# Optimization experiments

Hardware: AMD Instinct MI355X
Metric: run time of the kernel (lower is better)

## Reference

```python
import jax, jax.numpy as jnp
import numpy as np

N = 50000      # nodes
E = 800000     # edges
IN = 16        # node_features_size
OUT = 32       # conv out channels
HID = 25       # edge-MLP hidden
C = 10         # num_classes


def setup_inputs() -> dict:
    key = jax.random.key(0)
    ks = jax.random.split(key, 12)
    inp = {
        "x": jax.random.normal(ks[0], (N, IN), dtype=jnp.float32),
        "edge_attr": jax.random.uniform(ks[1], (E, 1), dtype=jnp.float32),
        "edge_index": jax.random.randint(ks[2], (2, E), 0, N, dtype=jnp.int64),
        # edge-MLP nn1: Linear(1,25) -> ReLU -> Linear(25, IN*OUT)
        "w1": jax.random.normal(ks[3], (1, HID), dtype=jnp.float32) * (1.0 / np.sqrt(1)),
        "b1": jnp.zeros((HID,), dtype=jnp.float32),
        "w2": jax.random.normal(ks[4], (HID, IN * OUT), dtype=jnp.float32) * (1.0 / np.sqrt(HID)),
        "b2": jnp.zeros((IN * OUT,), dtype=jnp.float32),
        # NNConv root weight and bias
        "root": jax.random.normal(ks[5], (IN, OUT), dtype=jnp.float32) * (1.0 / np.sqrt(IN)),
        "bias": jnp.zeros((OUT,), dtype=jnp.float32),
        # fc1: Linear(32, C)
        "fc_w": jax.random.normal(ks[6], (OUT, C), dtype=jnp.float32) * (1.0 / np.sqrt(OUT)),
        "fc_b": jnp.zeros((C,), dtype=jnp.float32),
    }
    return inp


def reference(x, edge_attr, edge_index, w1, b1, w2, b2, root, bias, fc_w, fc_b):
    src = edge_index[0]  # message sources (x_j)
    dst = edge_index[1]  # aggregation targets (x_i)
    # edge MLP -> per-edge weight matrices [E, IN, OUT]
    h = jax.nn.relu(edge_attr @ w1 + b1)
    w_e = (h @ w2 + b2).reshape(-1, IN, OUT)
    # gather source features, per-edge matmul
    msg = jnp.einsum('ei,eio->eo', x[src], w_e)  # [E, OUT]
    # scatter-max aggregation to destination nodes
    agg = jax.ops.segment_max(msg, dst, num_segments=N)
    agg = jnp.where(jnp.isfinite(agg), agg, 0.0)  # empty segments -> 0
    # root transform + bias, then ELU and classifier
    out = jax.nn.elu(agg + x @ root + bias)
    logits = out @ fc_w + fc_b
    return jax.nn.log_softmax(logits, axis=1)
```

## Files before the change

kernel.cpp:

```cpp
#include <hip/hip_runtime.h>
#include <hip/hip_bf16.h>
#include <stdint.h>

#define NN   50000
#define NE   800000
#define INF_ 16
#define OUTF 32
#define HIDN 25
#define NC   10
#define QG   2048
#define QPB  16
#define DPB  16
#define NB   3125
#define EPB  4096
#define NBLK 196
#define ASTR 33
#define ECAP 768
#define SCH  13

#define SENT 0x007FFFFFu

#define GB_PQ   98
#define GB_HIST NBLK
#define GB_G2   128
#define GB_XH   391

typedef _Float16 f16x2 __attribute__((ext_vector_type(2)));

__device__ __forceinline__ uint32_t map_f(float f) {
    uint32_t b = __float_as_uint(f);
    return (b & 0x80000000u) ? ~b : (b | 0x80000000u);
}
__device__ __forceinline__ float unmap_f(uint32_t u) {
    return (u & 0x80000000u) ? __uint_as_float(u ^ 0x80000000u)
                             : __uint_as_float(~u);
}
__device__ __forceinline__ float f16lo(uint32_t u) {
    union { uint16_t s; _Float16 h; } v; v.s = (uint16_t)(u & 0xFFFF);
    return (float)v.h;
}
__device__ __forceinline__ float f16hi(uint32_t u) {
    union { uint16_t s; _Float16 h; } v; v.s = (uint16_t)(u >> 16);
    return (float)v.h;
}
__device__ __forceinline__ uint32_t packf16(float a, float b) {
    union { uint32_t u; f16x2 h; } p;
    p.h[0] = (_Float16)a; p.h[1] = (_Float16)b;
    return p.u;
}
__device__ __forceinline__ float dot2f(uint32_t g, uint32_t xb, float acc) {
#if __has_builtin(__builtin_amdgcn_fdot2)
    union { uint32_t u; f16x2 h; } ug, ux;
    ug.u = g; ux.u = xb;
    return __builtin_amdgcn_fdot2(ug.h, ux.h, acc, false);
#else
    return fmaf(f16lo(g), f16lo(xb), fmaf(f16hi(g), f16hi(xb), acc));
#endif
}

__global__ __launch_bounds__(64) void flag_k(const float* __restrict__ w1,
                                             const float* __restrict__ b1,
                                             uint32_t* __restrict__ flagw) {
    if (threadIdx.x == 0) {
        uint32_t flag = 1, mask = 0;
        for (int k = 0; k < HIDN; ++k) {
            float w = w1[k], b = b1[k];
            if (w != 0.f) {
                float t = -b / w;
                if (t > 0.f && t < 1.f) flag = 0;
            }
            if (fmaf(0.5f, w, b) > 0.f) mask |= (1u << k);
        }
        flagw[0] = flag;
        flagw[1] = mask;
    }
}

__global__ __launch_bounds__(256) void prep_k(const float* __restrict__ w1,
                                              const float* __restrict__ b1,
                                              const float* __restrict__ w2,
                                              const float* __restrict__ b2,
                                              const float* __restrict__ x,
                                              const int* __restrict__ ei,
                                              const uint32_t* __restrict__ flagw,
                                              uint32_t* __restrict__ PQ,
                                              uint32_t* __restrict__ G2,
                                              uint32_t* __restrict__ xh,
                                              uint32_t* __restrict__ H) {
    __shared__ union {
        struct {
            float w2s[HIDN * 512];
            float b2s[512];
            float ca[512];
            float cb[512];
            float hs[QPB][HIDN];
        } g;
        uint32_t hloc[NB];
    } sm;

    const int b = blockIdx.x;
    if (b < GB_PQ) {
        for (int i = threadIdx.x; i < HIDN * 512; i += 256) sm.g.w2s[i] = w2[i];
        for (int i = threadIdx.x; i < 512; i += 256) sm.g.b2s[i] = b2[i];
        __syncthreads();
        const uint32_t mask = flagw[1];
        for (int e = threadIdx.x; e < 512; e += 256) {
            float ca = sm.g.b2s[e], cb = 0.f;
            for (int k = 0; k < HIDN; ++k) {
                if ((mask >> k) & 1u) {
                    float wv = sm.g.w2s[k * 512 + e];
                    ca = fmaf(b1[k], wv, ca);
                    cb = fmaf(w1[k], wv, cb);
                }
            }
            sm.g.ca[e] = ca;
            sm.g.cb[e] = cb;
        }
        __syncthreads();
        for (int rep = 0; rep < 2; ++rep) {
            int n = b * 512 + rep * 256 + threadIdx.x;
            if (n < NN) {
                float xv[INF_];
                const float* xr = x + (size_t)n * INF_;
#pragma unroll
                for (int i = 0; i < INF_; i += 4) {
                    float4 v = *reinterpret_cast<const float4*>(xr + i);
                    xv[i] = v.x; xv[i+1] = v.y; xv[i+2] = v.z; xv[i+3] = v.w;
                }
                float P[OUTF], Q[OUTF];
#pragma unroll
                for (int o = 0; o < OUTF; ++o) {
                    float p = 0.f, q = 0.f;
#pragma unroll
                    for (int i = 0; i < INF_; ++i) {
                        p = fmaf(xv[i], sm.g.ca[i * 32 + o], p);
                        q = fmaf(xv[i], sm.g.cb[i * 32 + o], q);
                    }
                    P[o] = p; Q[o] = q;
                }
                uint32_t* row = PQ + (size_t)n * 32;
#pragma unroll
                for (int j = 0; j < 16; ++j) row[j] = packf16(P[2*j], P[2*j+1]);
#pragma unroll
                for (int j = 0; j < 16; ++j) row[16+j] = packf16(Q[2*j], Q[2*j+1]);
            }
        }
    } else if (b < GB_PQ + GB_HIST) {
        const int blk = b - GB_PQ;
        for (int i = threadIdx.x; i < NB; i += 256) sm.hloc[i] = 0;
        __syncthreads();
        const int base = blk * EPB;
        for (int j = 0; j < EPB; j += 256) {
            int e = base + j + threadIdx.x;
            if (e < NE) atomicAdd(&sm.hloc[ei[NE + e] >> 4], 1u);
        }
        __syncthreads();
        for (int i = threadIdx.x; i < NB; i += 256)
            H[(size_t)i * NBLK + blk] = sm.hloc[i];
    } else if (b < GB_PQ + GB_HIST + GB_G2) {
        if (flagw[0] == 1u) return;
        const int gb = b - GB_PQ - GB_HIST;
        for (int i = threadIdx.x; i < HIDN * 512; i += 256) sm.g.w2s[i] = w2[i];
        for (int i = threadIdx.x; i < 512; i += 256) sm.g.b2s[i] = b2[i];
        for (int i = threadIdx.x; i < QPB * HIDN; i += 256) {
            int qq = i / HIDN, k = i - qq * HIDN;
            float aq = (gb * QPB + qq + 0.5f) * (1.0f / (float)QG);
            sm.g.hs[qq][k] = fmaxf(fmaf(aq, w1[k], b1[k]), 0.f);
        }
        __syncthreads();
        for (int qq = 0; qq < QPB; ++qq) {
            const int q = gb * QPB + qq;
            int e = threadIdx.x;
            int ip = e >> 5, o = e & 31;
            float g0 = sm.g.b2s[(2 * ip) * OUTF + o];
            float g1 = sm.g.b2s[(2 * ip + 1) * OUTF + o];
#pragma unroll
            for (int k = 0; k < HIDN; ++k) {
                float h = sm.g.hs[qq][k];
                g0 = fmaf(h, sm.g.w2s[k * 512 + (2 * ip) * OUTF + o], g0);
                g1 = fmaf(h, sm.g.w2s[k * 512 + (2 * ip + 1) * OUTF + o], g1);
            }
            G2[(size_t)q * 256 + e] = packf16(g0, g1);
        }
    } else {
        if (flagw[0] == 1u) return;
        int t4 = ((b - GB_PQ - GB_HIST - GB_G2) * 256 + threadIdx.x) * 4;
        if (t4 < NN * INF_ / 2) {
            const float4* xp = reinterpret_cast<const float4*>(x) + (t4 >> 1);
            float4 va = xp[0];
            float4 vb = xp[1];
            xh[t4]     = packf16(va.x, va.y);
            xh[t4 + 1] = packf16(va.z, va.w);
            xh[t4 + 2] = packf16(vb.x, vb.y);
            xh[t4 + 3] = packf16(vb.z, vb.w);
        }
    }
}

__global__ __launch_bounds__(256) void colsum_k(const uint32_t* __restrict__ H,
                                                uint32_t* __restrict__ Bp,
                                                uint32_t* __restrict__ tot) {
    const int bin  = (blockIdx.x * 256 + threadIdx.x) >> 6;
    const int lane = threadIdx.x & 63;
    if (bin >= NB) return;
    const uint32_t* hr = H + (size_t)bin * NBLK;
    uint32_t* br = Bp + (size_t)bin * NBLK;
    uint32_t carry = 0;
    for (int b0 = 0; b0 < NBLK; b0 += 64) {
        int b = b0 + lane;
        uint32_t v = (b < NBLK) ? hr[b] : 0;
        uint32_t inc = v;
#pragma unroll
        for (int off = 1; off < 64; off <<= 1) {
            uint32_t t = __shfl_up(inc, off);
            if (lane >= off) inc += t;
        }
        if (b < NBLK) br[b] = carry + inc - v;
        carry += __shfl(inc, 63);
    }
    if (lane == 0) tot[bin] = carry;
}

__global__ __launch_bounds__(256) void binscan_k(const uint32_t* __restrict__ tot,
                                                 uint32_t* __restrict__ bstart) {
    __shared__ uint32_t part[256];
    const int t = threadIdx.x;
    uint32_t loc[SCH];
    uint32_t s = 0;
#pragma unroll
    for (int j = 0; j < SCH; ++j) {
        int idx = t * SCH + j;
        uint32_t v = (idx < NB) ? tot[idx] : 0;
        loc[j] = s;
        s += v;
    }
    part[t] = s;
    __syncthreads();
    for (int off = 1; off < 256; off <<= 1) {
        uint32_t add = (t >= off) ? part[t - off] : 0;
        __syncthreads();
        part[t] += add;
        __syncthreads();
    }
    uint32_t base = (t > 0) ? part[t - 1] : 0;
#pragma unroll
    for (int j = 0; j < SCH; ++j) {
        int idx = t * SCH + j;
        if (idx < NB) bstart[idx] = base + loc[j];
    }
    if (t == 255) bstart[NB] = part[255];
}

__global__ __launch_bounds__(256) void scatter_k(const int* __restrict__ ei,
                                                 const float* __restrict__ ea,
                                                 const uint32_t* __restrict__ Bp,
                                                 const uint32_t* __restrict__ bstart,
                                                 uint2* __restrict__ sorted) {
    __shared__ uint32_t cur[NB];
    for (int i = threadIdx.x; i < NB; i += 256) cur[i] = 0;
    __syncthreads();
    const int base = blockIdx.x * EPB;
    for (int j = 0; j < EPB; j += 256) {
        int e = base + j + threadIdx.x;
        if (e < NE) {
            int sn = ei[e];
            int d  = ei[NE + e];
            float a = ea[e];
            int bin = d >> 4;
            uint32_t r = atomicAdd(&cur[bin], 1u);
            uint32_t pos = bstart[bin] + Bp[(size_t)bin * NBLK + blockIdx.x] + r;
            sorted[pos] = make_uint2(__float_as_uint(a),
                                     ((uint32_t)sn << 4) | (uint32_t)(d & 15));
        }
    }
}

__global__ __launch_bounds__(256) void fused_k(const uint2* __restrict__ sorted,
                                               const uint32_t* __restrict__ bstart,
                                               const uint32_t* __restrict__ flagw,
                                               const float* __restrict__ x,
                                               const uint32_t* __restrict__ PQ,
                                               const uint32_t* __restrict__ xh,
                                               const uint32_t* __restrict__ G2,
                                               const float* __restrict__ root,
                                               const float* __restrict__ bias,
                                               const float* __restrict__ fcw,
                                               const float* __restrict__ fcb,
                                               float* __restrict__ out) {
    __shared__ uint2    ebuf[ECAP];
    __shared__ uint32_t agg[DPB * ASTR];
    __shared__ float rs[INF_ * OUTF];
    __shared__ float bs[OUTF];
    __shared__ float fws[OUTF * NC];
    __shared__ float fbs[NC];

    const int bin  = blockIdx.x;
    const int segs = (int)bstart[bin];
    const int cnt  = (int)bstart[bin + 1] - segs;
    const int scnt = cnt < ECAP ? cnt : ECAP;

    for (int i = threadIdx.x; i < scnt; i += 256) ebuf[i] = sorted[segs + i];
    for (int i = threadIdx.x; i < DPB * ASTR; i += 256) agg[i] = SENT;
    for (int i = threadIdx.x; i < INF_ * OUTF; i += 256) rs[i] = root[i];
    if (threadIdx.x < OUTF) bs[threadIdx.x] = bias[threadIdx.x];
    for (int i = threadIdx.x; i < OUTF * NC; i += 256) fws[i] = fcw[i];
    if (threadIdx.x < NC) fbs[threadIdx.x] = fcb[threadIdx.x];
    const uint32_t flag = flagw[0];
    __syncthreads();

    const int c   = threadIdx.x & 7;
    const int grp = threadIdx.x >> 3;

    if (flag) {
        int it = grp;
        for (; it + 32 < cnt; it += 64) {
            uint2 rA = (it < ECAP) ? ebuf[it] : sorted[segs + it];
            int itB = it + 32;
            uint2 rB = (itB < ECAP) ? ebuf[itB] : sorted[segs + itB];
            float aA = __uint_as_float(rA.x), aB = __uint_as_float(rB.x);
            int sA = rA.y >> 4, sB = rB.y >> 4;
            int dA = rA.y & 15, dB = rB.y & 15;
            const uint2* pA = reinterpret_cast<const uint2*>(PQ + (size_t)sA * 32);
            const uint2* pB = reinterpret_cast<const uint2*>(PQ + (size_t)sB * 32);
            uint2 PuA = pA[c], QuA = pA[8 + c];
            uint2 PuB = pB[c], QuB = pB[8 + c];

            float a0 = fmaf(aA, f16lo(QuA.x), f16lo(PuA.x));
            float a1 = fmaf(aA, f16hi(QuA.x), f16hi(PuA.x));
            float a2 = fmaf(aA, f16lo(QuA.y), f16lo(PuA.y));
            float a3 = fmaf(aA, f16hi(QuA.y), f16hi(PuA.y));
            float b0 = fmaf(aB, f16lo(QuB.x), f16lo(PuB.x));
            float b1v = fmaf(aB, f16hi(QuB.x), f16hi(PuB.x));
            float b2v = fmaf(aB, f16lo(QuB.y), f16lo(PuB.y));
            float b3 = fmaf(aB, f16hi(QuB.y), f16hi(PuB.y));

            uint32_t* agA = &agg[dA * ASTR + c * 4];
            atomicMax(&agA[0], map_f(a0));
            atomicMax(&agA[1], map_f(a1));
            atomicMax(&agA[2], map_f(a2));
            atomicMax(&agA[3], map_f(a3));
            uint32_t* agB = &agg[dB * ASTR + c * 4];
            atomicMax(&agB[0], map_f(b0));
            atomicMax(&agB[1], map_f(b1v));
            atomicMax(&agB[2], map_f(b2v));
            atomicMax(&agB[3], map_f(b3));
        }
        if (it < cnt) {
            uint2 rA = (it < ECAP) ? ebuf[it] : sorted[segs + it];
            float aA = __uint_as_float(rA.x);
            int sA = rA.y >> 4;
            int dA = rA.y & 15;
            const uint2* pA = reinterpret_cast<const uint2*>(PQ + (size_t)sA * 32);
            uint2 PuA = pA[c], QuA = pA[8 + c];
            float a0 = fmaf(aA, f16lo(QuA.x), f16lo(PuA.x));
            float a1 = fmaf(aA, f16hi(QuA.x), f16hi(PuA.x));
            float a2 = fmaf(aA, f16lo(QuA.y), f16lo(PuA.y));
            float a3 = fmaf(aA, f16hi(QuA.y), f16hi(PuA.y));
            uint32_t* agA = &agg[dA * ASTR + c * 4];
            atomicMax(&agA[0], map_f(a0));
            atomicMax(&agA[1], map_f(a1));
            atomicMax(&agA[2], map_f(a2));
            atomicMax(&agA[3], map_f(a3));
        }
    } else {
        for (int it = grp; it < cnt; it += 32) {
            uint2 rec = (it < ECAP) ? ebuf[it] : sorted[segs + it];
            float a = __uint_as_float(rec.x);
            int src = rec.y >> 4;
            int db  = rec.y & 15;
            int q = (int)(a * (float)QG);
            q = q < 0 ? 0 : (q > QG - 1 ? QG - 1 : q);
            const uint4* xp = reinterpret_cast<const uint4*>(xh) + src * 2;
            uint4 hx0 = xp[0];
            uint4 hx1 = xp[1];
            const uint4* gq = reinterpret_cast<const uint4*>(G2) + (size_t)q * 64 + c;
            uint4 g0 = gq[0],  g1 = gq[8],  g2 = gq[16], g3 = gq[24];
            uint4 g4 = gq[32], g5 = gq[40], g6 = gq[48], g7 = gq[56];
            float p0 = 0.f, p1 = 0.f, p2 = 0.f, p3 = 0.f;
            p0 = dot2f(g0.x, hx0.x, p0); p1 = dot2f(g0.y, hx0.x, p1);
            p2 = dot2f(g0.z, hx0.x, p2); p3 = dot2f(g0.w, hx0.x, p3);
            p0 = dot2f(g1.x, hx0.y, p0); p1 = dot2f(g1.y, hx0.y, p1);
            p2 = dot2f(g1.z, hx0.y, p2); p3 = dot2f(g1.w, hx0.y, p3);
            p0 = dot2f(g2.x, hx0.z, p0); p1 = dot2f(g2.y, hx0.z, p1);
            p2 = dot2f(g2.z, hx0.z, p2); p3 = dot2f(g2.w, hx0.z, p3);
            p0 = dot2f(g3.x, hx0.w, p0); p1 = dot2f(g3.y, hx0.w, p1);
            p2 = dot2f(g3.z, hx0.w, p2); p3 = dot2f(g3.w, hx0.w, p3);
            p0 = dot2f(g4.x, hx1.x, p0); p1 = dot2f(g4.y, hx1.x, p1);
            p2 = dot2f(g4.z, hx1.x, p2); p3 = dot2f(g4.w, hx1.x, p3);
            p0 = dot2f(g5.x, hx1.y, p0); p1 = dot2f(g5.y, hx1.y, p1);
            p2 = dot2f(g5.z, hx1.y, p2); p3 = dot2f(g5.w, hx1.y, p3);
            p0 = dot2f(g6.x, hx1.z, p0); p1 = dot2f(g6.y, hx1.z, p1);
            p2 = dot2f(g6.z, hx1.z, p2); p3 = dot2f(g6.w, hx1.z, p3);
            p0 = dot2f(g7.x, hx1.w, p0); p1 = dot2f(g7.y, hx1.w, p1);
            p2 = dot2f(g7.z, hx1.w, p2); p3 = dot2f(g7.w, hx1.w, p3);
            uint32_t* ag = &agg[db * ASTR + c * 4];
            atomicMax(&ag[0], map_f(p0));
            atomicMax(&ag[1], map_f(p1));
            atomicMax(&ag[2], map_f(p2));
            atomicMax(&ag[3], map_f(p3));
        }
    }
    __syncthreads();

    {
        const int li8 = threadIdx.x & 7;
        const int dl  = threadIdx.x >> 3;
        const int n   = bin * DPB + dl;
        if (dl < DPB && n < NN) {
            const uint32_t* ar = &agg[dl * ASTR + li8 * 4];
            float av[4];
#pragma unroll
            for (int qq = 0; qq < 4; ++qq) {
                uint32_t u = ar[qq];
                av[qq] = (u == SENT) ? 0.f : unmap_f(u);
            }
            const float* xr = x + (size_t)n * INF_;
            float4 xa = *reinterpret_cast<const float4*>(xr);
            float4 xb = *reinterpret_cast<const float4*>(xr + 4);
            float4 xc = *reinterpret_cast<const float4*>(xr + 8);
            float4 xd = *reinterpret_cast<const float4*>(xr + 12);
            float xv[INF_] = {xa.x,xa.y,xa.z,xa.w, xb.x,xb.y,xb.z,xb.w,
                              xc.x,xc.y,xc.z,xc.w, xd.x,xd.y,xd.z,xd.w};
            float ov[4];
#pragma unroll
            for (int qq = 0; qq < 4; ++qq) {
                int oc = li8 * 4 + qq;
                float tv = av[qq] + bs[oc];
#pragma unroll
                for (int i = 0; i < INF_; ++i) tv = fmaf(xv[i], rs[i * OUTF + oc], tv);
                ov[qq] = (tv > 0.f) ? tv : expm1f(tv);
            }
            float lg[NC];
#pragma unroll
            for (int cc = 0; cc < NC; ++cc) {
                float tv = 0.f;
#pragma unroll
                for (int qq = 0; qq < 4; ++qq) tv = fmaf(ov[qq], fws[(li8 * 4 + qq) * NC + cc], tv);
                lg[cc] = tv;
            }
#pragma unroll
            for (int m = 1; m <= 4; m <<= 1) {
#pragma unroll
                for (int cc = 0; cc < NC; ++cc) lg[cc] += __shfl_xor(lg[cc], m);
            }
#pragma unroll
            for (int cc = 0; cc < NC; ++cc) lg[cc] += fbs[cc];

            float mx = lg[0];
#pragma unroll
            for (int cc = 1; cc < NC; ++cc) mx = fmaxf(mx, lg[cc]);
            float ssum = 0.f;
#pragma unroll
            for (int cc = 0; cc < NC; ++cc) ssum += expf(lg[cc] - mx);
            float lse = mx + logf(ssum);

            float* orow = out + (size_t)n * NC;
            orow[li8] = lg[li8] - lse;
            if (li8 < 2) orow[8 + li8] = lg[8 + li8] - lse;
        }
    }
}

extern "C" void kernel_launch(void* const* d_in, const int* in_sizes, int n_in,
                              void* d_out, int out_size, void* d_ws, size_t ws_size,
                              hipStream_t stream) {
    const float* x    = (const float*)d_in[0];
    const float* ea   = (const float*)d_in[1];
    const int*   ei   = (const int*)d_in[2];
    const float* w1   = (const float*)d_in[3];
    const float* b1   = (const float*)d_in[4];
    const float* w2   = (const float*)d_in[5];
    const float* b2   = (const float*)d_in[6];
    const float* root = (const float*)d_in[7];
    const float* bias = (const float*)d_in[8];
    const float* fcw  = (const float*)d_in[9];
    const float* fcb  = (const float*)d_in[10];
    float* out = (float*)d_out;

    size_t off = 0;
    auto alloc = [&](size_t bytes) {
        void* p = (char*)d_ws + off;
        off += (bytes + 255) & ~(size_t)255;
        return p;
    };
    uint32_t* flagw    = (uint32_t*)alloc(256);
    uint32_t* PQ       = (uint32_t*)alloc((size_t)NN * 32 * 4);
    uint32_t* G2       = (uint32_t*)alloc((size_t)QG * 256 * 4);
    uint32_t* xh       = (uint32_t*)alloc((size_t)NN * INF_ * 2);
    uint32_t* H        = (uint32_t*)alloc((size_t)NB * NBLK * 4);
    uint32_t* Bp       = (uint32_t*)alloc((size_t)NB * NBLK * 4);
    uint32_t* tot      = (uint32_t*)alloc((size_t)NB * 4);
    uint32_t* bstart   = (uint32_t*)alloc((size_t)(NB + 1) * 4);
    uint2*    sorted   = (uint2*)alloc((size_t)NE * 8);

    flag_k<<<1, 64, 0, stream>>>(w1, b1, flagw);
    prep_k<<<GB_PQ + GB_HIST + GB_G2 + GB_XH, 256, 0, stream>>>(
        w1, b1, w2, b2, x, ei, flagw, PQ, G2, xh, H);
    colsum_k<<<(NB * 64 + 255) / 256, 256, 0, stream>>>(H, Bp, tot);
    binscan_k<<<1, 256, 0, stream>>>(tot, bstart);
    scatter_k<<<NBLK, 256, 0, stream>>>(ei, ea, Bp, bstart, sorted);
    fused_k<<<NB, 256, 0, stream>>>(sorted, bstart, flagw, x, PQ, xh, G2,
                                    root, bias, fcw, fcb, out);
}
```

Before: 86.78 us.

## Inline flag computation, drop flag kernel, and spread PQ precompute over more blocks

```diff
diff --git a/kernel.cpp b/kernel.cpp
--- a/kernel.cpp
+++ b/kernel.cpp
@@ -20,7 +20,7 @@
 
 #define SENT 0x007FFFFFu
 
-#define GB_PQ   98
+#define GB_PQ   1563
 #define GB_HIST NBLK
 #define GB_G2   128
 #define GB_XH   391
@@ -58,22 +58,16 @@
 #endif
 }
 
-__global__ __launch_bounds__(64) void flag_k(const float* __restrict__ w1,
-                                             const float* __restrict__ b1,
-                                             uint32_t* __restrict__ flagw) {
-    if (threadIdx.x == 0) {
-        uint32_t flag = 1, mask = 0;
-        for (int k = 0; k < HIDN; ++k) {
-            float w = w1[k], b = b1[k];
-            if (w != 0.f) {
-                float t = -b / w;
-                if (t > 0.f && t < 1.f) flag = 0;
-            }
-            if (fmaf(0.5f, w, b) > 0.f) mask |= (1u << k);
-        }
-        flagw[0] = flag;
-        flagw[1] = mask;
-    }
+__device__ __forceinline__ uint32_t calc_flag(const float* w1, const float* b1) {
+    uint32_t flag = 1;
+    for (int k = 0; k < HIDN; ++k) {
+        float w = w1[k], b = b1[k];
+        if (w != 0.f) {
+            float t = -b / w;
+            if (t > 0.f && t < 1.f) flag = 0;
+        }
+    }
+    return flag;
 }
 
 __global__ __launch_bounds__(256) void prep_k(const float* __restrict__ w1,
@@ -82,68 +76,61 @@
                                               const float* __restrict__ b2,
                                               const float* __restrict__ x,
                                               const int* __restrict__ ei,
-                                              const uint32_t* __restrict__ flagw,
                                               uint32_t* __restrict__ PQ,
                                               uint32_t* __restrict__ G2,
                                               uint32_t* __restrict__ xh,
                                               uint32_t* __restrict__ H) {
     __shared__ union {
-        struct {
-            float w2s[HIDN * 512];
-            float b2s[512];
-            float ca[512];
-            float cb[512];
-            float hs[QPB][HIDN];
-        } g;
+        struct { float ca[512]; float cb[512]; } pq;
         uint32_t hloc[NB];
+        float hs[QPB][HIDN];
     } sm;
 
     const int b = blockIdx.x;
     if (b < GB_PQ) {
-        for (int i = threadIdx.x; i < HIDN * 512; i += 256) sm.g.w2s[i] = w2[i];
-        for (int i = threadIdx.x; i < 512; i += 256) sm.g.b2s[i] = b2[i];
-        __syncthreads();
-        const uint32_t mask = flagw[1];
+        uint32_t mask = 0;
+        for (int k = 0; k < HIDN; ++k)
+            if (fmaf(0.5f, w1[k], b1[k]) > 0.f) mask |= (1u << k);
         for (int e = threadIdx.x; e < 512; e += 256) {
-            float ca = sm.g.b2s[e], cb = 0.f;
+            float ca = b2[e], cb = 0.f;
             for (int k = 0; k < HIDN; ++k) {
                 if ((mask >> k) & 1u) {
-                    float wv = sm.g.w2s[k * 512 + e];
+                    float wv = w2[k * 512 + e];
                     ca = fmaf(b1[k], wv, ca);
                     cb = fmaf(w1[k], wv, cb);
                 }
             }
-            sm.g.ca[e] = ca;
-            sm.g.cb[e] = cb;
-        }
-        __syncthreads();
-        for (int rep = 0; rep < 2; ++rep) {
-            int n = b * 512 + rep * 256 + threadIdx.x;
-            if (n < NN) {
-                float xv[INF_];
-                const float* xr = x + (size_t)n * INF_;
-#pragma unroll
-                for (int i = 0; i < INF_; i += 4) {
-                    float4 v = *reinterpret_cast<const float4*>(xr + i);
-                    xv[i] = v.x; xv[i+1] = v.y; xv[i+2] = v.z; xv[i+3] = v.w;
+            sm.pq.ca[e] = ca;
+            sm.pq.cb[e] = cb;
+        }
+        __syncthreads();
+        const int c = threadIdx.x & 7;
+        const int n = b * 32 + (threadIdx.x >> 3);
+        if (n < NN) {
+            float xv[INF_];
+            const float* xr = x + (size_t)n * INF_;
+#pragma unroll
+            for (int i = 0; i < INF_; i += 4) {
+                float4 v = *reinterpret_cast<const float4*>(xr + i);
+                xv[i] = v.x; xv[i+1] = v.y; xv[i+2] = v.z; xv[i+3] = v.w;
+            }
+            float P[4], Q[4];
+#pragma unroll
+            for (int j = 0; j < 4; ++j) {
+                int o = c * 4 + j;
+                float p = 0.f, q = 0.f;
+#pragma unroll
+                for (int i = 0; i < INF_; ++i) {
+                    p = fmaf(xv[i], sm.pq.ca[i * 32 + o], p);
+                    q = fmaf(xv[i], sm.pq.cb[i * 32 + o], q);
                 }
-                float P[OUTF], Q[OUTF];
-#pragma unroll
-                for (int o = 0; o < OUTF; ++o) {
-                    float p = 0.f, q = 0.f;
-#pragma unroll
-                    for (int i = 0; i < INF_; ++i) {
-                        p = fmaf(xv[i], sm.g.ca[i * 32 + o], p);
-                        q = fmaf(xv[i], sm.g.cb[i * 32 + o], q);
-                    }
-                    P[o] = p; Q[o] = q;
-                }
-                uint32_t* row = PQ + (size_t)n * 32;
-#pragma unroll
-                for (int j = 0; j < 16; ++j) row[j] = packf16(P[2*j], P[2*j+1]);
-#pragma unroll
-                for (int j = 0; j < 16; ++j) row[16+j] = packf16(Q[2*j], Q[2*j+1]);
-            }
+                P[j] = p; Q[j] = q;
+            }
+            uint32_t* row = PQ + (size_t)n * 32;
+            row[2*c]      = packf16(P[0], P[1]);
+            row[2*c + 1]  = packf16(P[2], P[3]);
+            row[16 + 2*c]     = packf16(Q[0], Q[1]);
+            row[16 + 2*c + 1] = packf16(Q[2], Q[3]);
         }
     } else if (b < GB_PQ + GB_HIST) {
         const int blk = b - GB_PQ;
@@ -158,32 +145,30 @@
         for (int i = threadIdx.x; i < NB; i += 256)
             H[(size_t)i * NBLK + blk] = sm.hloc[i];
     } else if (b < GB_PQ + GB_HIST + GB_G2) {
-        if (flagw[0] == 1u) return;
+        if (calc_flag(w1, b1)) return;
         const int gb = b - GB_PQ - GB_HIST;
-        for (int i = threadIdx.x; i < HIDN * 512; i += 256) sm.g.w2s[i] = w2[i];
-        for (int i = threadIdx.x; i < 512; i += 256) sm.g.b2s[i] = b2[i];
         for (int i = threadIdx.x; i < QPB * HIDN; i += 256) {
             int qq = i / HIDN, k = i - qq * HIDN;
             float aq = (gb * QPB + qq + 0.5f) * (1.0f / (float)QG);
-            sm.g.hs[qq][k] = fmaxf(fmaf(aq, w1[k], b1[k]), 0.f);
+            sm.hs[qq][k] = fmaxf(fmaf(aq, w1[k], b1[k]), 0.f);
         }
         __syncthreads();
         for (int qq = 0; qq < QPB; ++qq) {
             const int q = gb * QPB + qq;
             int e = threadIdx.x;
             int ip = e >> 5, o = e & 31;
-            float g0 = sm.g.b2s[(2 * ip) * OUTF + o];
-            float g1 = sm.g.b2s[(2 * ip + 1) * OUTF + o];
+            float g0 = b2[(2 * ip) * OUTF + o];
+            float g1 = b2[(2 * ip + 1) * OUTF + o];
 #pragma unroll
             for (int k = 0; k < HIDN; ++k) {
-                float h = sm.g.hs[qq][k];
-                g0 = fmaf(h, sm.g.w2s[k * 512 + (2 * ip) * OUTF + o], g0);
-                g1 = fmaf(h, sm.g.w2s[k * 512 + (2 * ip + 1) * OUTF + o], g1);
+                float h = sm.hs[qq][k];
+                g0 = fmaf(h, w2[k * 512 + (2 * ip) * OUTF + o], g0);
+                g1 = fmaf(h, w2[k * 512 + (2 * ip + 1) * OUTF + o], g1);
             }
             G2[(size_t)q * 256 + e] = packf16(g0, g1);
         }
     } else {
-        if (flagw[0] == 1u) return;
+        if (calc_flag(w1, b1)) return;
         int t4 = ((b - GB_PQ - GB_HIST - GB_G2) * 256 + threadIdx.x) * 4;
         if (t4 < NN * INF_ / 2) {
             const float4* xp = reinterpret_cast<const float4*>(x) + (t4 >> 1);
@@ -277,7 +262,8 @@
 
 __global__ __launch_bounds__(256) void fused_k(const uint2* __restrict__ sorted,
                                                const uint32_t* __restrict__ bstart,
-                                               const uint32_t* __restrict__ flagw,
+                                               const float* __restrict__ w1,
+                                               const float* __restrict__ b1,
                                                const float* __restrict__ x,
                                                const uint32_t* __restrict__ PQ,
                                                const uint32_t* __restrict__ xh,
@@ -305,7 +291,7 @@
     if (threadIdx.x < OUTF) bs[threadIdx.x] = bias[threadIdx.x];
     for (int i = threadIdx.x; i < OUTF * NC; i += 256) fws[i] = fcw[i];
     if (threadIdx.x < NC) fbs[threadIdx.x] = fcb[threadIdx.x];
-    const uint32_t flag = flagw[0];
+    const uint32_t flag = calc_flag(w1, b1);
     __syncthreads();
 
     const int c   = threadIdx.x & 7;
@@ -483,7 +469,6 @@
         off += (bytes + 255) & ~(size_t)255;
         return p;
     };
-    uint32_t* flagw    = (uint32_t*)alloc(256);
     uint32_t* PQ       = (uint32_t*)alloc((size_t)NN * 32 * 4);
     uint32_t* G2       = (uint32_t*)alloc((size_t)QG * 256 * 4);
     uint32_t* xh       = (uint32_t*)alloc((size_t)NN * INF_ * 2);
@@ -493,12 +478,11 @@
     uint32_t* bstart   = (uint32_t*)alloc((size_t)(NB + 1) * 4);
     uint2*    sorted   = (uint2*)alloc((size_t)NE * 8);
 
-    flag_k<<<1, 64, 0, stream>>>(w1, b1, flagw);
     prep_k<<<GB_PQ + GB_HIST + GB_G2 + GB_XH, 256, 0, stream>>>(
-        w1, b1, w2, b2, x, ei, flagw, PQ, G2, xh, H);
+        w1, b1, w2, b2, x, ei, PQ, G2, xh, H);
     colsum_k<<<(NB * 64 + 255) / 256, 256, 0, stream>>>(H, Bp, tot);
     binscan_k<<<1, 256, 0, stream>>>(tot, bstart);
     scatter_k<<<NBLK, 256, 0, stream>>>(ei, ea, Bp, bstart, sorted);
-    fused_k<<<NB, 256, 0, stream>>>(sorted, bstart, flagw, x, PQ, xh, G2,
+    fused_k<<<NB, 256, 0, stream>>>(sorted, bstart, w1, b1, x, PQ, xh, G2,
                                     root, bias, fcw, fcb, out);
 }
```

Result: faster. 81.69 us (-5.9%).
